# Kernel tuning notes

Hardware: AMD Instinct MI355X
Metric: run time of the kernel (lower is better)

The kernel has to match this reference:

```python
import jax, jax.numpy as jnp
import numpy as np

B, SQ, SK, DIM, HEADS, DH = 2, 1024, 1024, 512, 1, 64
INNER = HEADS * DH  # 64


def setup_inputs() -> dict:
    key = jax.random.key(0)
    ks = jax.random.split(key, 7)
    s = 0.05
    return {
        "x": jax.random.normal(ks[0], (B, SQ, DIM), jnp.float32),
        "emb": jax.random.normal(ks[1], (B, SK, DIM), jnp.float32),
        "Wq": jax.random.normal(ks[2], (DIM, INNER), jnp.float32) * s,
        "Wk": jax.random.normal(ks[3], (DIM, INNER), jnp.float32) * s,
        "Wv": jax.random.normal(ks[4], (DIM, INNER), jnp.float32) * s,
        "Wo": jax.random.normal(ks[5], (INNER, DIM), jnp.float32) * s,
        "bo": jnp.zeros((DIM,), jnp.float32),
    }


def reference(x, emb, Wq, Wk, Wv, Wo, bo):
    # QKV projections (bias-free Dense layers)
    q = x @ Wq     # [B, SQ, INNER]
    k = emb @ Wk   # [B, SK, INNER]
    v = emb @ Wv   # [B, SK, INNER]
    # Faithful to the module's reshape: (B, -1, inner_dim, heads).
    # With heads=1 the attention sees num_heads=INNER and q_features=heads=1.
    q = q.reshape(q.shape[0], -1, q.shape[-1], HEADS)  # [B, SQ, INNER, 1]
    k = k.reshape(k.shape[0], -1, k.shape[-1], HEADS)  # [B, SK, INNER, 1]
    v = v.reshape(v.shape[0], -1, v.shape[-1], HEADS)  # [B, SK, INNER, 1]
    # Memory-efficient attention scales q by q_features**-0.5 (here =1)
    scale = jnp.asarray(q.shape[-1], q.dtype) ** -0.5
    s = jnp.einsum('bqhd,bkhd->bqhk', q * scale, k)    # [B, SQ, INNER, SK]
    p = jax.nn.softmax(s, axis=-1)
    o = jnp.einsum('bqhk,bkhd->bqhd', p, v)            # [B, SQ, INNER, 1]
    o = o.reshape(x.shape[0], x.shape[1], -1)          # [B, SQ, INNER]
    return o @ Wo + bo                                 # [B, SQ, DIM]
```

## Files before the change

### kernel.cpp

```cpp
#include <hip/hip_runtime.h>
#include <hip/hip_bf16.h>

#define LOG2E 1.44269504088896340736f

__device__ __forceinline__ float fast_exp2(float x) {
#if __has_builtin(__builtin_amdgcn_exp2f)
    return __builtin_amdgcn_exp2f(x);
#else
    return exp2f(x);
#endif
}

__global__ __launch_bounds__(256) void proj_kernel(
    const float* __restrict__ x, const float* __restrict__ emb,
    const float* __restrict__ Wq, const float* __restrict__ Wk,
    const float* __restrict__ Wv,
    float* __restrict__ qT, float* __restrict__ kT, float* __restrict__ vT)
{
    __shared__ __align__(16) float sx[4096];
    __shared__ __align__(16) float sred[4096];
    const int t   = threadIdx.x;
    const int bid = blockIdx.x;
    const bool isQ = (bid < 256);
    const int rb  = isQ ? bid : (bid - 256);

    const float* src = (isQ ? x : emb) + (size_t)rb * 8 * 512;
    #pragma unroll
    for (int i = 0; i < 16; ++i) sx[i * 256 + t] = src[i * 256 + t];
    __syncthreads();

    const int b  = rb >> 7;
    const int q0 = (rb << 3) & 1023;

    if (isQ) {
        const int cp = (t & 31) * 2;
        const int g  = t >> 5;
        const int d0 = g * 64;
        float acc0[8], acc1[8];
        #pragma unroll
        for (int r = 0; r < 8; ++r) { acc0[r] = 0.f; acc1[r] = 0.f; }
        for (int dd = 0; dd < 64; dd += 4) {
            const int d = d0 + dd;
            float2 w0 = *(const float2*)&Wq[(d + 0) * 64 + cp];
            float2 w1 = *(const float2*)&Wq[(d + 1) * 64 + cp];
            float2 w2 = *(const float2*)&Wq[(d + 2) * 64 + cp];
            float2 w3 = *(const float2*)&Wq[(d + 3) * 64 + cp];
            #pragma unroll
            for (int r = 0; r < 8; ++r) {
                float4 xv = *(const float4*)&sx[r * 512 + d];
                acc0[r] = fmaf(xv.x, w0.x, acc0[r]); acc1[r] = fmaf(xv.x, w0.y, acc1[r]);
                acc0[r] = fmaf(xv.y, w1.x, acc0[r]); acc1[r] = fmaf(xv.y, w1.y, acc1[r]);
                acc0[r] = fmaf(xv.z, w2.x, acc0[r]); acc1[r] = fmaf(xv.z, w2.y, acc1[r]);
                acc0[r] = fmaf(xv.w, w3.x, acc0[r]); acc1[r] = fmaf(xv.w, w3.y, acc1[r]);
            }
        }
        #pragma unroll
        for (int r = 0; r < 8; ++r)
            *(float2*)&sred[g * 512 + r * 64 + cp] = make_float2(acc0[r], acc1[r]);
        __syncthreads();
        #pragma unroll
        for (int p = 0; p < 2; ++p) {
            int idx = p * 256 + t;
            int r = idx >> 6, h = idx & 63;
            float s = 0.f;
            #pragma unroll
            for (int g2 = 0; g2 < 8; ++g2) s += sred[g2 * 512 + r * 64 + h];
            qT[(size_t)(b * 64 + h) * 1024 + q0 + r] = s;
        }
    } else {
        const int cp = (t & 63) * 2;
        const int g  = t >> 6;
        const int d0 = g * 128;
        const float* Wsel = (cp < 64) ? (Wk + cp) : (Wv + (cp - 64));
        float acc0[8], acc1[8];
        #pragma unroll
        for (int r = 0; r < 8; ++r) { acc0[r] = 0.f; acc1[r] = 0.f; }
        for (int dd = 0; dd < 128; dd += 4) {
            const int d = d0 + dd;
            float2 w0 = *(const float2*)&Wsel[(d + 0) * 64];
            float2 w1 = *(const float2*)&Wsel[(d + 1) * 64];
            float2 w2 = *(const float2*)&Wsel[(d + 2) * 64];
            float2 w3 = *(const float2*)&Wsel[(d + 3) * 64];
            #pragma unroll
            for (int r = 0; r < 8; ++r) {
                float4 xv = *(const float4*)&sx[r * 512 + d];
                acc0[r] = fmaf(xv.x, w0.x, acc0[r]); acc1[r] = fmaf(xv.x, w0.y, acc1[r]);
                acc0[r] = fmaf(xv.y, w1.x, acc0[r]); acc1[r] = fmaf(xv.y, w1.y, acc1[r]);
                acc0[r] = fmaf(xv.z, w2.x, acc0[r]); acc1[r] = fmaf(xv.z, w2.y, acc1[r]);
                acc0[r] = fmaf(xv.w, w3.x, acc0[r]); acc1[r] = fmaf(xv.w, w3.y, acc1[r]);
            }
        }
        #pragma unroll
        for (int r = 0; r < 8; ++r)
            *(float2*)&sred[g * 1024 + r * 128 + cp] = make_float2(acc0[r], acc1[r]);
        __syncthreads();
        #pragma unroll
        for (int p = 0; p < 4; ++p) {
            int idx = p * 256 + t;
            int r = idx >> 7, c = idx & 127;
            float s = 0.f;
            #pragma unroll
            for (int g2 = 0; g2 < 4; ++g2) s += sred[g2 * 1024 + r * 128 + c];
            if (c < 64) kT[(size_t)(b * 64 + c) * 1024 + q0 + r] = s;
            else        vT[(size_t)(b * 64 + (c - 64)) * 1024 + q0 + r] = s;
        }
    }
}

__global__ __launch_bounds__(256) void attn_kernel(
    const float* __restrict__ qT, const float* __restrict__ kT,
    const float* __restrict__ vT, float* __restrict__ O)
{
    __shared__ __align__(16) float kc[1024];
    __shared__ __align__(16) float vc[1024];
    __shared__ float wred[8];
    const int t   = threadIdx.x;
    const int bid = blockIdx.x;
    const int b   = bid >> 8;
    const int h   = (bid >> 2) & 63;
    const int qc  = bid & 3;
    const size_t base = (size_t)(b * 64 + h) * 1024;

    float kmx = -1e30f, kmn = 1e30f;
    #pragma unroll
    for (int i = 0; i < 4; ++i) {
        float kv = kT[base + i * 256 + t];
        float vv = vT[base + i * 256 + t];
        kc[i * 256 + t] = kv;
        vc[i * 256 + t] = vv;
        kmx = fmaxf(kmx, kv);
        kmn = fminf(kmn, kv);
    }
    #pragma unroll
    for (int off = 32; off >= 1; off >>= 1) {
        kmx = fmaxf(kmx, __shfl_xor(kmx, off));
        kmn = fminf(kmn, __shfl_xor(kmn, off));
    }
    const int wid = t >> 6;
    if ((t & 63) == 0) { wred[wid] = kmx; wred[4 + wid] = kmn; }
    __syncthreads();
    kmx = fmaxf(fmaxf(wred[0], wred[1]), fmaxf(wred[2], wred[3]));
    kmn = fminf(fminf(wred[4], wred[5]), fminf(wred[6], wred[7]));

    const float qs = qT[base + qc * 256 + t];
    const float m  = (qs >= 0.f) ? qs * kmx : qs * kmn;
    const float a  = qs * LOG2E;
    const float bb = -m * LOG2E;

    float d0 = 0.f, d1 = 0.f, d2 = 0.f, d3 = 0.f;
    float n0 = 0.f, n1 = 0.f, n2 = 0.f, n3 = 0.f;
    const float4* kc4 = (const float4*)kc;
    const float4* vc4 = (const float4*)vc;
    for (int j = 0; j < 256; ++j) {
        float4 k4 = kc4[j];
        float4 v4 = vc4[j];
        float e0 = fast_exp2(fmaf(a, k4.x, bb));
        float e1 = fast_exp2(fmaf(a, k4.y, bb));
        float e2 = fast_exp2(fmaf(a, k4.z, bb));
        float e3 = fast_exp2(fmaf(a, k4.w, bb));
        d0 += e0; n0 = fmaf(e0, v4.x, n0);
        d1 += e1; n1 = fmaf(e1, v4.y, n1);
        d2 += e2; n2 = fmaf(e2, v4.z, n2);
        d3 += e3; n3 = fmaf(e3, v4.w, n3);
    }
    const float den = (d0 + d1) + (d2 + d3);
    const float num = (n0 + n1) + (n2 + n3);
    const int q = qc * 256 + t;
    O[(size_t)(b * 1024 + q) * 64 + h] = num / den;
}

__global__ __launch_bounds__(256) void oproj_kernel(
    const float* __restrict__ O, const float* __restrict__ Wo,
    const float* __restrict__ bo, float* __restrict__ out)
{
    __shared__ __align__(16) float so[512];
    const int t  = threadIdx.x;
    const int rb = blockIdx.x;
    const size_t r0 = (size_t)rb * 8;
    so[t]       = O[r0 * 64 + t];
    so[t + 256] = O[r0 * 64 + t + 256];
    __syncthreads();

    const int d2 = t * 2;
    float2 bv = *(const float2*)&bo[d2];
    float acc0[8], acc1[8];
    #pragma unroll
    for (int r = 0; r < 8; ++r) { acc0[r] = bv.x; acc1[r] = bv.y; }
    for (int hh = 0; hh < 64; hh += 4) {
        float2 w0 = *(const float2*)&Wo[(hh + 0) * 512 + d2];
        float2 w1 = *(const float2*)&Wo[(hh + 1) * 512 + d2];
        float2 w2 = *(const float2*)&Wo[(hh + 2) * 512 + d2];
        float2 w3 = *(const float2*)&Wo[(hh + 3) * 512 + d2];
        #pragma unroll
        for (int r = 0; r < 8; ++r) {
            float4 s4 = *(const float4*)&so[r * 64 + hh];
            acc0[r] = fmaf(s4.x, w0.x, acc0[r]); acc1[r] = fmaf(s4.x, w0.y, acc1[r]);
            acc0[r] = fmaf(s4.y, w1.x, acc0[r]); acc1[r] = fmaf(s4.y, w1.y, acc1[r]);
            acc0[r] = fmaf(s4.z, w2.x, acc0[r]); acc1[r] = fmaf(s4.z, w2.y, acc1[r]);
            acc0[r] = fmaf(s4.w, w3.x, acc0[r]); acc1[r] = fmaf(s4.w, w3.y, acc1[r]);
        }
    }
    #pragma unroll
    for (int r = 0; r < 8; ++r)
        *(float2*)&out[(r0 + r) * 512 + d2] = make_float2(acc0[r], acc1[r]);
}

extern "C" void kernel_launch(void* const* d_in, const int* in_sizes, int n_in,
                              void* d_out, int out_size, void* d_ws, size_t ws_size,
                              hipStream_t stream)
{
    const float* x   = (const float*)d_in[0];
    const float* emb = (const float*)d_in[1];
    const float* Wq  = (const float*)d_in[2];
    const float* Wk  = (const float*)d_in[3];
    const float* Wv  = (const float*)d_in[4];
    const float* Wo  = (const float*)d_in[5];
    const float* bo  = (const float*)d_in[6];
    float* out = (float*)d_out;

    float* qT = (float*)d_ws;
    float* kT = qT + 131072;
    float* vT = kT + 131072;
    float* O  = vT + 131072;

    proj_kernel<<<512, 256, 0, stream>>>(x, emb, Wq, Wk, Wv, qT, kT, vT);
    attn_kernel<<<512, 256, 0, stream>>>(qT, kT, vT, O);
    oproj_kernel<<<256, 256, 0, stream>>>(O, Wo, bo, out);
}
```

Before: 109.9 us.

## Fuse projection, attention and output kernels into one cooperative launch

Merges the three kernels into one persistent cooperative kernel of 512 blocks, with grid-wide syncs between the QKV projection, attention and output projection phases. It shares one 32KB LDS buffer across the phases and reshapes the output projection to 4 rows per block so all 512 blocks take part. The goal is to cut the launch overhead and inter-kernel gaps of three small kernels. In exchange it adds grid.sync costs and needs all 512 blocks co-resident, so occupancy is capped at two blocks per CU.

```diff
diff --git a/kernel.cpp b/kernel.cpp
--- a/kernel.cpp
+++ b/kernel.cpp
@@ -1,5 +1,7 @@
 #include <hip/hip_runtime.h>
-#include <hip/hip_bf16.h>
+#include <hip/hip_cooperative_groups.h>
+
+namespace cg = cooperative_groups;
 
 #define LOG2E 1.44269504088896340736f
 
@@ -11,198 +13,198 @@
 #endif
 }
 
-__global__ __launch_bounds__(256) void proj_kernel(
+__global__ __launch_bounds__(256, 2) void fused_kernel(
     const float* __restrict__ x, const float* __restrict__ emb,
     const float* __restrict__ Wq, const float* __restrict__ Wk,
-    const float* __restrict__ Wv,
-    float* __restrict__ qT, float* __restrict__ kT, float* __restrict__ vT)
+    const float* __restrict__ Wv, const float* __restrict__ Wo,
+    const float* __restrict__ bo, float* __restrict__ out,
+    float* __restrict__ qT, float* __restrict__ kT,
+    float* __restrict__ vT, float* __restrict__ O)
 {
-    __shared__ __align__(16) float sx[4096];
-    __shared__ __align__(16) float sred[4096];
+    __shared__ __align__(16) float smem[8192];
     const int t   = threadIdx.x;
     const int bid = blockIdx.x;
-    const bool isQ = (bid < 256);
-    const int rb  = isQ ? bid : (bid - 256);
-
-    const float* src = (isQ ? x : emb) + (size_t)rb * 8 * 512;
-    #pragma unroll
-    for (int i = 0; i < 16; ++i) sx[i * 256 + t] = src[i * 256 + t];
-    __syncthreads();
-
-    const int b  = rb >> 7;
-    const int q0 = (rb << 3) & 1023;
-
-    if (isQ) {
-        const int cp = (t & 31) * 2;
-        const int g  = t >> 5;
-        const int d0 = g * 64;
-        float acc0[8], acc1[8];
-        #pragma unroll
-        for (int r = 0; r < 8; ++r) { acc0[r] = 0.f; acc1[r] = 0.f; }
-        for (int dd = 0; dd < 64; dd += 4) {
-            const int d = d0 + dd;
-            float2 w0 = *(const float2*)&Wq[(d + 0) * 64 + cp];
-            float2 w1 = *(const float2*)&Wq[(d + 1) * 64 + cp];
-            float2 w2 = *(const float2*)&Wq[(d + 2) * 64 + cp];
-            float2 w3 = *(const float2*)&Wq[(d + 3) * 64 + cp];
-            #pragma unroll
-            for (int r = 0; r < 8; ++r) {
-                float4 xv = *(const float4*)&sx[r * 512 + d];
-                acc0[r] = fmaf(xv.x, w0.x, acc0[r]); acc1[r] = fmaf(xv.x, w0.y, acc1[r]);
-                acc0[r] = fmaf(xv.y, w1.x, acc0[r]); acc1[r] = fmaf(xv.y, w1.y, acc1[r]);
-                acc0[r] = fmaf(xv.z, w2.x, acc0[r]); acc1[r] = fmaf(xv.z, w2.y, acc1[r]);
-                acc0[r] = fmaf(xv.w, w3.x, acc0[r]); acc1[r] = fmaf(xv.w, w3.y, acc1[r]);
-            }
-        }
-        #pragma unroll
-        for (int r = 0; r < 8; ++r)
-            *(float2*)&sred[g * 512 + r * 64 + cp] = make_float2(acc0[r], acc1[r]);
+    cg::grid_group grid = cg::this_grid();
+
+    {
+        float* sx   = smem;
+        float* sred = smem + 4096;
+        const bool isQ = (bid < 256);
+        const int rb  = isQ ? bid : (bid - 256);
+
+        const float* src = (isQ ? x : emb) + (size_t)rb * 8 * 512;
+        #pragma unroll
+        for (int i = 0; i < 16; ++i) sx[i * 256 + t] = src[i * 256 + t];
         __syncthreads();
-        #pragma unroll
-        for (int p = 0; p < 2; ++p) {
-            int idx = p * 256 + t;
-            int r = idx >> 6, h = idx & 63;
-            float s = 0.f;
-            #pragma unroll
-            for (int g2 = 0; g2 < 8; ++g2) s += sred[g2 * 512 + r * 64 + h];
-            qT[(size_t)(b * 64 + h) * 1024 + q0 + r] = s;
-        }
-    } else {
-        const int cp = (t & 63) * 2;
-        const int g  = t >> 6;
-        const int d0 = g * 128;
-        const float* Wsel = (cp < 64) ? (Wk + cp) : (Wv + (cp - 64));
-        float acc0[8], acc1[8];
-        #pragma unroll
-        for (int r = 0; r < 8; ++r) { acc0[r] = 0.f; acc1[r] = 0.f; }
-        for (int dd = 0; dd < 128; dd += 4) {
-            const int d = d0 + dd;
-            float2 w0 = *(const float2*)&Wsel[(d + 0) * 64];
-            float2 w1 = *(const float2*)&Wsel[(d + 1) * 64];
-            float2 w2 = *(const float2*)&Wsel[(d + 2) * 64];
-            float2 w3 = *(const float2*)&Wsel[(d + 3) * 64];
-            #pragma unroll
-            for (int r = 0; r < 8; ++r) {
-                float4 xv = *(const float4*)&sx[r * 512 + d];
-                acc0[r] = fmaf(xv.x, w0.x, acc0[r]); acc1[r] = fmaf(xv.x, w0.y, acc1[r]);
-                acc0[r] = fmaf(xv.y, w1.x, acc0[r]); acc1[r] = fmaf(xv.y, w1.y, acc1[r]);
-                acc0[r] = fmaf(xv.z, w2.x, acc0[r]); acc1[r] = fmaf(xv.z, w2.y, acc1[r]);
-                acc0[r] = fmaf(xv.w, w3.x, acc0[r]); acc1[r] = fmaf(xv.w, w3.y, acc1[r]);
-            }
-        }
-        #pragma unroll
-        for (int r = 0; r < 8; ++r)
-            *(float2*)&sred[g * 1024 + r * 128 + cp] = make_float2(acc0[r], acc1[r]);
+
+        const int b  = rb >> 7;
+        const int q0 = (rb << 3) & 1023;
+
+        if (isQ) {
+            const int cp = (t & 31) * 2;
+            const int g  = t >> 5;
+            const int d0 = g * 64;
+            float acc0[8], acc1[8];
+            #pragma unroll
+            for (int r = 0; r < 8; ++r) { acc0[r] = 0.f; acc1[r] = 0.f; }
+            for (int dd = 0; dd < 64; dd += 4) {
+                const int d = d0 + dd;
+                float2 w0 = *(const float2*)&Wq[(d + 0) * 64 + cp];
+                float2 w1 = *(const float2*)&Wq[(d + 1) * 64 + cp];
+                float2 w2 = *(const float2*)&Wq[(d + 2) * 64 + cp];
+                float2 w3 = *(const float2*)&Wq[(d + 3) * 64 + cp];
+                #pragma unroll
+                for (int r = 0; r < 8; ++r) {
+                    float4 xv = *(const float4*)&sx[r * 512 + d];
+                    acc0[r] = fmaf(xv.x, w0.x, acc0[r]); acc1[r] = fmaf(xv.x, w0.y, acc1[r]);
+                    acc0[r] = fmaf(xv.y, w1.x, acc0[r]); acc1[r] = fmaf(xv.y, w1.y, acc1[r]);
+                    acc0[r] = fmaf(xv.z, w2.x, acc0[r]); acc1[r] = fmaf(xv.z, w2.y, acc1[r]);
+                    acc0[r] = fmaf(xv.w, w3.x, acc0[r]); acc1[r] = fmaf(xv.w, w3.y, acc1[r]);
+                }
+            }
+            #pragma unroll
+            for (int r = 0; r < 8; ++r)
+                *(float2*)&sred[g * 512 + r * 64 + cp] = make_float2(acc0[r], acc1[r]);
+            __syncthreads();
+            #pragma unroll
+            for (int p = 0; p < 2; ++p) {
+                int idx = p * 256 + t;
+                int r = idx >> 6, h = idx & 63;
+                float s = 0.f;
+                #pragma unroll
+                for (int g2 = 0; g2 < 8; ++g2) s += sred[g2 * 512 + r * 64 + h];
+                qT[(size_t)(b * 64 + h) * 1024 + q0 + r] = s;
+            }
+        } else {
+            const int cp = (t & 63) * 2;
+            const int g  = t >> 6;
+            const int d0 = g * 128;
+            const float* Wsel = (cp < 64) ? (Wk + cp) : (Wv + (cp - 64));
+            float acc0[8], acc1[8];
+            #pragma unroll
+            for (int r = 0; r < 8; ++r) { acc0[r] = 0.f; acc1[r] = 0.f; }
+            for (int dd = 0; dd < 128; dd += 4) {
+                const int d = d0 + dd;
+                float2 w0 = *(const float2*)&Wsel[(d + 0) * 64];
+                float2 w1 = *(const float2*)&Wsel[(d + 1) * 64];
+                float2 w2 = *(const float2*)&Wsel[(d + 2) * 64];
+                float2 w3 = *(const float2*)&Wsel[(d + 3) * 64];
+                #pragma unroll
+                for (int r = 0; r < 8; ++r) {
+                    float4 xv = *(const float4*)&sx[r * 512 + d];
+                    acc0[r] = fmaf(xv.x, w0.x, acc0[r]); acc1[r] = fmaf(xv.x, w0.y, acc1[r]);
+                    acc0[r] = fmaf(xv.y, w1.x, acc0[r]); acc1[r] = fmaf(xv.y, w1.y, acc1[r]);
+                    acc0[r] = fmaf(xv.z, w2.x, acc0[r]); acc1[r] = fmaf(xv.z, w2.y, acc1[r]);
+                    acc0[r] = fmaf(xv.w, w3.x, acc0[r]); acc1[r] = fmaf(xv.w, w3.y, acc1[r]);
+                }
+            }
+            #pragma unroll
+            for (int r = 0; r < 8; ++r)
+                *(float2*)&sred[g * 1024 + r * 128 + cp] = make_float2(acc0[r], acc1[r]);
+            __syncthreads();
+            #pragma unroll
+            for (int p = 0; p < 4; ++p) {
+                int idx = p * 256 + t;
+                int r = idx >> 7, c = idx & 127;
+                float s = 0.f;
+                #pragma unroll
+                for (int g2 = 0; g2 < 4; ++g2) s += sred[g2 * 1024 + r * 128 + c];
+                if (c < 64) kT[(size_t)(b * 64 + c) * 1024 + q0 + r] = s;
+                else        vT[(size_t)(b * 64 + (c - 64)) * 1024 + q0 + r] = s;
+            }
+        }
+    }
+
+    grid.sync();
+
+    {
+        float* kc   = smem;
+        float* vc   = smem + 1024;
+        float* wred = smem + 2048;
+        const int b  = bid >> 8;
+        const int h  = (bid >> 2) & 63;
+        const int qc = bid & 3;
+        const size_t base = (size_t)(b * 64 + h) * 1024;
+
+        float kmx = -1e30f, kmn = 1e30f;
+        #pragma unroll
+        for (int i = 0; i < 4; ++i) {
+            float kv = kT[base + i * 256 + t];
+            float vv = vT[base + i * 256 + t];
+            kc[i * 256 + t] = kv;
+            vc[i * 256 + t] = vv;
+            kmx = fmaxf(kmx, kv);
+            kmn = fminf(kmn, kv);
+        }
+        #pragma unroll
+        for (int off = 32; off >= 1; off >>= 1) {
+            kmx = fmaxf(kmx, __shfl_xor(kmx, off));
+            kmn = fminf(kmn, __shfl_xor(kmn, off));
+        }
+        const int wid = t >> 6;
+        if ((t & 63) == 0) { wred[wid] = kmx; wred[4 + wid] = kmn; }
         __syncthreads();
-        #pragma unroll
-        for (int p = 0; p < 4; ++p) {
-            int idx = p * 256 + t;
-            int r = idx >> 7, c = idx & 127;
-            float s = 0.f;
-            #pragma unroll
-            for (int g2 = 0; g2 < 4; ++g2) s += sred[g2 * 1024 + r * 128 + c];
-            if (c < 64) kT[(size_t)(b * 64 + c) * 1024 + q0 + r] = s;
-            else        vT[(size_t)(b * 64 + (c - 64)) * 1024 + q0 + r] = s;
-        }
+        kmx = fmaxf(fmaxf(wred[0], wred[1]), fmaxf(wred[2], wred[3]));
+        kmn = fminf(fminf(wred[4], wred[5]), fminf(wred[6], wred[7]));
+
+        const float qs = qT[base + qc * 256 + t];
+        const float m  = (qs >= 0.f) ? qs * kmx : qs * kmn;
+        const float a  = qs * LOG2E;
+        const float bb = -m * LOG2E;
+
+        float d0 = 0.f, d1 = 0.f, d2 = 0.f, d3 = 0.f;
+        float n0 = 0.f, n1 = 0.f, n2 = 0.f, n3 = 0.f;
+        const float4* kc4 = (const float4*)kc;
+        const float4* vc4 = (const float4*)vc;
+        for (int j = 0; j < 256; ++j) {
+            float4 k4 = kc4[j];
+            float4 v4 = vc4[j];
+            float e0 = fast_exp2(fmaf(a, k4.x, bb));
+            float e1 = fast_exp2(fmaf(a, k4.y, bb));
+            float e2 = fast_exp2(fmaf(a, k4.z, bb));
+            float e3 = fast_exp2(fmaf(a, k4.w, bb));
+            d0 += e0; n0 = fmaf(e0, v4.x, n0);
+            d1 += e1; n1 = fmaf(e1, v4.y, n1);
+            d2 += e2; n2 = fmaf(e2, v4.z, n2);
+            d3 += e3; n3 = fmaf(e3, v4.w, n3);
+        }
+        const float den = (d0 + d1) + (d2 + d3);
+        const float num = (n0 + n1) + (n2 + n3);
+        const int q = qc * 256 + t;
+        O[(size_t)(b * 1024 + q) * 64 + h] = num / den;
     }
-}
-
-__global__ __launch_bounds__(256) void attn_kernel(
-    const float* __restrict__ qT, const float* __restrict__ kT,
-    const float* __restrict__ vT, float* __restrict__ O)
-{
-    __shared__ __align__(16) float kc[1024];
-    __shared__ __align__(16) float vc[1024];
-    __shared__ float wred[8];
-    const int t   = threadIdx.x;
-    const int bid = blockIdx.x;
-    const int b   = bid >> 8;
-    const int h   = (bid >> 2) & 63;
-    const int qc  = bid & 3;
-    const size_t base = (size_t)(b * 64 + h) * 1024;
-
-    float kmx = -1e30f, kmn = 1e30f;
-    #pragma unroll
-    for (int i = 0; i < 4; ++i) {
-        float kv = kT[base + i * 256 + t];
-        float vv = vT[base + i * 256 + t];
-        kc[i * 256 + t] = kv;
-        vc[i * 256 + t] = vv;
-        kmx = fmaxf(kmx, kv);
-        kmn = fminf(kmn, kv);
+
+    grid.sync();
+
+    {
+        float* so = smem;
+        const size_t r0 = (size_t)bid * 4;
+        so[t] = O[r0 * 64 + t];
+        __syncthreads();
+
+        const int d2 = t * 2;
+        float2 bv = *(const float2*)&bo[d2];
+        float acc0[4], acc1[4];
+        #pragma unroll
+        for (int r = 0; r < 4; ++r) { acc0[r] = bv.x; acc1[r] = bv.y; }
+        for (int hh = 0; hh < 64; hh += 4) {
+            float2 w0 = *(const float2*)&Wo[(hh + 0) * 512 + d2];
+            float2 w1 = *(const float2*)&Wo[(hh + 1) * 512 + d2];
+            float2 w2 = *(const float2*)&Wo[(hh + 2) * 512 + d2];
+            float2 w3 = *(const float2*)&Wo[(hh + 3) * 512 + d2];
+            #pragma unroll
+            for (int r = 0; r < 4; ++r) {
+                float4 s4 = *(const float4*)&so[r * 64 + hh];
+                acc0[r] = fmaf(s4.x, w0.x, acc0[r]); acc1[r] = fmaf(s4.x, w0.y, acc1[r]);
+                acc0[r] = fmaf(s4.y, w1.x, acc0[r]); acc1[r] = fmaf(s4.y, w1.y, acc1[r]);
+                acc0[r] = fmaf(s4.z, w2.x, acc0[r]); acc1[r] = fmaf(s4.z, w2.y, acc1[r]);
+                acc0[r] = fmaf(s4.w, w3.x, acc0[r]); acc1[r] = fmaf(s4.w, w3.y, acc1[r]);
+            }
+        }
+        #pragma unroll
+        for (int r = 0; r < 4; ++r)
+            *(float2*)&out[(r0 + r) * 512 + d2] = make_float2(acc0[r], acc1[r]);
     }
-    #pragma unroll
-    for (int off = 32; off >= 1; off >>= 1) {
-        kmx = fmaxf(kmx, __shfl_xor(kmx, off));
-        kmn = fminf(kmn, __shfl_xor(kmn, off));
-    }
-    const int wid = t >> 6;
-    if ((t & 63) == 0) { wred[wid] = kmx; wred[4 + wid] = kmn; }
-    __syncthreads();
-    kmx = fmaxf(fmaxf(wred[0], wred[1]), fmaxf(wred[2], wred[3]));
-    kmn = fminf(fminf(wred[4], wred[5]), fminf(wred[6], wred[7]));
-
-    const float qs = qT[base + qc * 256 + t];
-    const float m  = (qs >= 0.f) ? qs * kmx : qs * kmn;
-    const float a  = qs * LOG2E;
-    const float bb = -m * LOG2E;
-
-    float d0 = 0.f, d1 = 0.f, d2 = 0.f, d3 = 0.f;
-    float n0 = 0.f, n1 = 0.f, n2 = 0.f, n3 = 0.f;
-    const float4* kc4 = (const float4*)kc;
-    const float4* vc4 = (const float4*)vc;
-    for (int j = 0; j < 256; ++j) {
-        float4 k4 = kc4[j];
-        float4 v4 = vc4[j];
-        float e0 = fast_exp2(fmaf(a, k4.x, bb));
-        float e1 = fast_exp2(fmaf(a, k4.y, bb));
-        float e2 = fast_exp2(fmaf(a, k4.z, bb));
-        float e3 = fast_exp2(fmaf(a, k4.w, bb));
-        d0 += e0; n0 = fmaf(e0, v4.x, n0);
-        d1 += e1; n1 = fmaf(e1, v4.y, n1);
-        d2 += e2; n2 = fmaf(e2, v4.z, n2);
-        d3 += e3; n3 = fmaf(e3, v4.w, n3);
-    }
-    const float den = (d0 + d1) + (d2 + d3);
-    const float num = (n0 + n1) + (n2 + n3);
-    const int q = qc * 256 + t;
-    O[(size_t)(b * 1024 + q) * 64 + h] = num / den;
-}
-
-__global__ __launch_bounds__(256) void oproj_kernel(
-    const float* __restrict__ O, const float* __restrict__ Wo,
-    const float* __restrict__ bo, float* __restrict__ out)
-{
-    __shared__ __align__(16) float so[512];
-    const int t  = threadIdx.x;
-    const int rb = blockIdx.x;
-    const size_t r0 = (size_t)rb * 8;
-    so[t]       = O[r0 * 64 + t];
-    so[t + 256] = O[r0 * 64 + t + 256];
-    __syncthreads();
-
-    const int d2 = t * 2;
-    float2 bv = *(const float2*)&bo[d2];
-    float acc0[8], acc1[8];
-    #pragma unroll
-    for (int r = 0; r < 8; ++r) { acc0[r] = bv.x; acc1[r] = bv.y; }
-    for (int hh = 0; hh < 64; hh += 4) {
-        float2 w0 = *(const float2*)&Wo[(hh + 0) * 512 + d2];
-        float2 w1 = *(const float2*)&Wo[(hh + 1) * 512 + d2];
-        float2 w2 = *(const float2*)&Wo[(hh + 2) * 512 + d2];
-        float2 w3 = *(const float2*)&Wo[(hh + 3) * 512 + d2];
-        #pragma unroll
-        for (int r = 0; r < 8; ++r) {
-            float4 s4 = *(const float4*)&so[r * 64 + hh];
-            acc0[r] = fmaf(s4.x, w0.x, acc0[r]); acc1[r] = fmaf(s4.x, w0.y, acc1[r]);
-            acc0[r] = fmaf(s4.y, w1.x, acc0[r]); acc1[r] = fmaf(s4.y, w1.y, acc1[r]);
-            acc0[r] = fmaf(s4.z, w2.x, acc0[r]); acc1[r] = fmaf(s4.z, w2.y, acc1[r]);
-            acc0[r] = fmaf(s4.w, w3.x, acc0[r]); acc1[r] = fmaf(s4.w, w3.y, acc1[r]);
-        }
-    }
-    #pragma unroll
-    for (int r = 0; r < 8; ++r)
-        *(float2*)&out[(r0 + r) * 512 + d2] = make_float2(acc0[r], acc1[r]);
 }
 
 extern "C" void kernel_launch(void* const* d_in, const int* in_sizes, int n_in,
@@ -223,7 +225,11 @@
     float* vT = kT + 131072;
     float* O  = vT + 131072;
 
-    proj_kernel<<<512, 256, 0, stream>>>(x, emb, Wq, Wk, Wv, qT, kT, vT);
-    attn_kernel<<<512, 256, 0, stream>>>(qT, kT, vT, O);
-    oproj_kernel<<<256, 256, 0, stream>>>(O, Wo, bo, out);
+    void* args[] = {
+        (void*)&x, (void*)&emb, (void*)&Wq, (void*)&Wk, (void*)&Wv,
+        (void*)&Wo, (void*)&bo, (void*)&out,
+        (void*)&qT, (void*)&kT, (void*)&vT, (void*)&O
+    };
+    hipLaunchCooperativeKernel((const void*)fused_kernel,
+                               dim3(512), dim3(256), args, 0, stream);
 }
```

Result: slower. 250.1 us (+127.6%).
